# Performance work log

Measured on AMD Instinct MI355X. Metric: run time of the kernel, lower is better.

Reference implementation:

```python
import jax, jax.numpy as jnp
import numpy as np

N_NODES = 50000
N_EDGES = 100000
NODE_IN = 64
EDGE_IN = 16
H = 32          # node_hidden_feats
EDGE_HID = 128  # edge_hidden_feats
STEPS = 6       # num_step_message_passing


def setup_inputs() -> dict:
    key = jax.random.key(0)
    ks = jax.random.split(key, 12)
    s = lambda k, *sh: jax.random.normal(k, sh, dtype=jnp.float32) * 0.05
    return {
        "node_ids": jax.random.randint(ks[0], (N_NODES,), 0, 343),
        "edge_ids": jax.random.randint(ks[1], (N_EDGES,), 0, 21),
        "src": jax.random.randint(ks[2], (N_EDGES,), 0, N_NODES),
        "dst": jax.random.randint(ks[3], (N_EDGES,), 0, N_NODES),
        "node_emb": s(ks[4], 343, NODE_IN),
        "edge_emb": s(ks[5], 21, EDGE_IN),
        "proj_W": s(ks[6], NODE_IN, H),
        "proj_b": jnp.zeros((H,), jnp.float32),
        "eW1": s(ks[7], EDGE_IN, EDGE_HID),
        "eb1": jnp.zeros((EDGE_HID,), jnp.float32),
        "eW2": s(ks[8], EDGE_HID, H * H),
        "eb2": jnp.zeros((H * H,), jnp.float32),
        "conv_bias": jnp.zeros((H,), jnp.float32),
        "gru_Wih": s(ks[9], 3 * H, H),
        "gru_Whh": s(ks[10], 3 * H, H),
        "gru_bih": jnp.zeros((3 * H,), jnp.float32),
        "gru_bhh": jnp.zeros((3 * H,), jnp.float32),
    }


def reference(node_ids, edge_ids, src, dst, node_emb, edge_emb, proj_W, proj_b,
              eW1, eb1, eW2, eb2, conv_bias, gru_Wih, gru_Whh, gru_bih, gru_bhh):
    # project node features
    h = jax.nn.relu(node_emb[node_ids] @ proj_W + proj_b)                 # [N, H]
    e = edge_emb[edge_ids]                                                # [E, EDGE_IN]
    # edge-conditioned weight matrices (edge feats are fixed, so identical every step)
    W_e = (jax.nn.relu(e @ eW1 + eb1) @ eW2 + eb2).reshape(N_EDGES, H, H)  # [E, H, H]
    hidden = h
    for _ in range(STEPS):
        # NNConv: gather src feats, per-edge matvec, scatter-sum to dst, + bias
        msg = jnp.einsum('ei,eio->eo', h[src], W_e)                        # [E, H]
        agg = jax.ops.segment_sum(msg, dst, num_segments=N_NODES) + conv_bias
        m = jax.nn.relu(agg)
        # GRU cell (PyTorch gate order: r, z, n)
        gi = m @ gru_Wih.T + gru_bih                                       # [N, 3H]
        gh = hidden @ gru_Whh.T + gru_bhh                                  # [N, 3H]
        ir, iz, inew = jnp.split(gi, 3, axis=-1)
        hr, hz, hnew = jnp.split(gh, 3, axis=-1)
        r = jax.nn.sigmoid(ir + hr)
        z = jax.nn.sigmoid(iz + hz)
        n = jnp.tanh(inew + r * hnew)
        hidden = (1.0 - z) * n + z * hidden
        h = hidden
    return h
```

## Files before the change

### kernel.cpp

```cpp
#include <hip/hip_runtime.h>

#define N_NODES 50000
#define N_EDGES 100000
#define NT 21
#define STEPS 6
#define BPT 40
#define NB 100
#define EPB 1000

__device__ __forceinline__ float sigm(float x) { return 1.f / (1.f + __expf(-x)); }
__device__ __forceinline__ float tanh_f(float x) {
    float t = __expf(2.f * fabsf(x));
    return copysignf(1.f - 2.f / (t + 1.f), x);
}

__global__ __launch_bounds__(256) void k_proj(const int* __restrict__ node_ids,
                                              const float* __restrict__ node_emb,
                                              const float* __restrict__ W,
                                              const float* __restrict__ b,
                                              float* __restrict__ h) {
    int lane = threadIdx.x & 31;
    int n = blockIdx.x * 8 + (threadIdx.x >> 5);
    if (n >= N_NODES) return;
    float w[64];
#pragma unroll
    for (int i = 0; i < 64; ++i) w[i] = W[i * 32 + lane];
    int id = node_ids[n];
    const float* er = node_emb + id * 64;
    float e0 = er[lane];
    float e1 = er[32 + lane];
    float acc = b[lane];
#pragma unroll
    for (int i = 0; i < 32; ++i) acc += __shfl(e0, i, 32) * w[i];
#pragma unroll
    for (int i = 0; i < 32; ++i) acc += __shfl(e1, i, 32) * w[32 + i];
    h[n * 32 + lane] = fmaxf(acc, 0.f);
}

__global__ __launch_bounds__(128) void k_wtable(const float* __restrict__ edge_emb,
                                                const float* __restrict__ eW1,
                                                const float* __restrict__ eb1,
                                                const float* __restrict__ eW2,
                                                const float* __restrict__ eb2,
                                                float* __restrict__ Wt) {
    __shared__ float x[128];
    int t = blockIdx.x >> 3, c = blockIdx.x & 7;
    int tid = threadIdx.x;
    float acc = eb1[tid];
#pragma unroll
    for (int i = 0; i < 16; ++i) acc += edge_emb[t * 16 + i] * eW1[i * 128 + tid];
    x[tid] = fmaxf(acc, 0.f);
    __syncthreads();
    int j = c * 128 + tid;
    float a = eb2[j];
#pragma unroll 8
    for (int i = 0; i < 128; ++i) a += x[i] * eW2[i * 1024 + j];
    Wt[t * 1024 + j] = a;
}

__global__ __launch_bounds__(256) void k_hist(const int* __restrict__ eid,
                                              int* __restrict__ hist) {
    __shared__ int lc[NT];
    if (threadIdx.x < NT) lc[threadIdx.x] = 0;
    __syncthreads();
    int e0 = blockIdx.x * EPB;
#pragma unroll
    for (int k = 0; k < EPB / 256 + 1; ++k) {
        int e = e0 + k * 256 + threadIdx.x;
        if (e < e0 + EPB) atomicAdd(&lc[eid[e]], 1);
    }
    __syncthreads();
    if (threadIdx.x < NT) hist[blockIdx.x * NT + threadIdx.x] = lc[threadIdx.x];
}

__global__ void k_offs(const int* __restrict__ hist,
                       int* __restrict__ offs,
                       int* __restrict__ cnt,
                       int* __restrict__ base) {
    __shared__ int tot[NT];
    int t = threadIdx.x;
    if (t < NT) {
        int run = 0;
        for (int b = 0; b < NB; ++b) { offs[b * NT + t] = run; run += hist[b * NT + t]; }
        tot[t] = run;
        cnt[t] = run;
    }
    __syncthreads();
    if (t == 0) {
        int r = 0;
        for (int tt = 0; tt < NT; ++tt) { base[tt] = r; r += tot[tt]; }
    }
}

__global__ __launch_bounds__(256) void k_fill2(const int* __restrict__ eid,
                                               const int* __restrict__ offs,
                                               const int* __restrict__ base,
                                               int* __restrict__ perm) {
    __shared__ int cur[NT];
    int b = blockIdx.x;
    if (threadIdx.x < NT) cur[threadIdx.x] = base[threadIdx.x] + offs[b * NT + threadIdx.x];
    __syncthreads();
    int e0 = b * EPB;
#pragma unroll
    for (int k = 0; k < EPB / 256 + 1; ++k) {
        int e = e0 + k * 256 + threadIdx.x;
        if (e < e0 + EPB) {
            int r = atomicAdd(&cur[eid[e]], 1);
            perm[r] = e;
        }
    }
}

__global__ __launch_bounds__(256) void k_msg(const int* __restrict__ perm,
                                             const int* __restrict__ base,
                                             const int* __restrict__ cnt,
                                             const int* __restrict__ src,
                                             const int* __restrict__ dst,
                                             const float* __restrict__ Wt,
                                             const float* __restrict__ h,
                                             float* __restrict__ agg) {
    int t = blockIdx.x / BPT, sub = blockIdx.x % BPT;
    int lane = threadIdx.x & 31, g = threadIdx.x >> 5;
    const float* wp = Wt + t * 1024;
    float w[32];
#pragma unroll
    for (int i = 0; i < 32; ++i) w[i] = wp[i * 32 + lane];
    int n = cnt[t], b0 = base[t];
    for (int idx = sub * 8 + g; idx < n; idx += BPT * 8) {
        int e = perm[b0 + idx];
        int s = src[e], d = dst[e];
        float hv = h[s * 32 + lane];
        float acc = 0.f;
#pragma unroll
        for (int i = 0; i < 32; ++i) acc += __shfl(hv, i, 32) * w[i];
        atomicAdd(&agg[d * 32 + lane], acc);
    }
}

__global__ __launch_bounds__(256) void k_gru(const float* __restrict__ Wih,
                                             const float* __restrict__ Whh,
                                             const float* __restrict__ bih,
                                             const float* __restrict__ bhh,
                                             const float* __restrict__ cb,
                                             float* __restrict__ agg,
                                             float* __restrict__ h) {
    __shared__ float wiT[32 * 96];
    __shared__ float whT[32 * 96];
    for (int u = threadIdx.x; u < 3072; u += 256) {
        int k = u >> 5, i = u & 31;
        wiT[i * 96 + k] = Wih[u];
        whT[i * 96 + k] = Whh[u];
    }
    __syncthreads();
    int gtid = blockIdx.x * 256 + threadIdx.x;
    int n = gtid >> 2, j = gtid & 3;
    if (n >= N_NODES) return;
    float* ap = agg + n * 32;
    float m[32], hv[32];
#pragma unroll
    for (int q = 0; q < 8; ++q) {
        float4 a = ((const float4*)ap)[q];
        float4 c = ((const float4*)cb)[q];
        m[4 * q + 0] = fmaxf(a.x + c.x, 0.f);
        m[4 * q + 1] = fmaxf(a.y + c.y, 0.f);
        m[4 * q + 2] = fmaxf(a.z + c.z, 0.f);
        m[4 * q + 3] = fmaxf(a.w + c.w, 0.f);
    }
#pragma unroll
    for (int q = 0; q < 8; ++q) {
        float4 x = ((const float4*)(h + n * 32))[q];
        hv[4 * q + 0] = x.x; hv[4 * q + 1] = x.y;
        hv[4 * q + 2] = x.z; hv[4 * q + 3] = x.w;
    }
    float4 z4 = make_float4(0.f, 0.f, 0.f, 0.f);
    ((float4*)ap)[2 * j] = z4;
    ((float4*)ap)[2 * j + 1] = z4;

    const int kb = j * 8;
    float acc[8];
#pragma unroll
    for (int q = 0; q < 8; ++q) acc[q] = 0.f;
#pragma unroll
    for (int i = 0; i < 32; ++i) {
        float mi = m[i], hi = hv[i];
        const float* wr = wiT + i * 96 + kb;
        const float* hr = whT + i * 96 + kb;
#pragma unroll
        for (int q = 0; q < 8; ++q) acc[q] += mi * wr[q] + hi * hr[q];
    }
    float rg[8];
#pragma unroll
    for (int q = 0; q < 8; ++q) rg[q] = sigm(acc[q] + bih[kb + q] + bhh[kb + q]);
    float aI[8], aH[8];
#pragma unroll
    for (int q = 0; q < 8; ++q) { aI[q] = 0.f; aH[q] = 0.f; }
#pragma unroll
    for (int i = 0; i < 32; ++i) {
        float mi = m[i], hi = hv[i];
        const float* wr = wiT + i * 96 + 64 + kb;
        const float* hr = whT + i * 96 + 64 + kb;
#pragma unroll
        for (int q = 0; q < 8; ++q) { aI[q] += mi * wr[q]; aH[q] += hi * hr[q]; }
    }
    float nn[8];
#pragma unroll
    for (int q = 0; q < 8; ++q)
        nn[q] = tanh_f(aI[q] + bih[64 + kb + q] + rg[q] * (aH[q] + bhh[64 + kb + q]));
#pragma unroll
    for (int q = 0; q < 8; ++q) acc[q] = 0.f;
#pragma unroll
    for (int i = 0; i < 32; ++i) {
        float mi = m[i], hi = hv[i];
        const float* wr = wiT + i * 96 + 32 + kb;
        const float* hr = whT + i * 96 + 32 + kb;
#pragma unroll
        for (int q = 0; q < 8; ++q) acc[q] += mi * wr[q] + hi * hr[q];
    }
    float out[8];
#pragma unroll
    for (int q = 0; q < 8; ++q) {
        float z = sigm(acc[q] + bih[32 + kb + q] + bhh[32 + kb + q]);
        out[q] = (1.f - z) * nn[q] + z * hv[kb + q];
    }
    float4 o0 = make_float4(out[0], out[1], out[2], out[3]);
    float4 o1 = make_float4(out[4], out[5], out[6], out[7]);
    ((float4*)(h + n * 32 + kb))[0] = o0;
    ((float4*)(h + n * 32 + kb))[1] = o1;
}

extern "C" void kernel_launch(void* const* d_in, const int* in_sizes, int n_in,
                              void* d_out, int out_size, void* d_ws, size_t ws_size,
                              hipStream_t stream) {
    const int*   node_ids  = (const int*)d_in[0];
    const int*   edge_ids  = (const int*)d_in[1];
    const int*   src       = (const int*)d_in[2];
    const int*   dst       = (const int*)d_in[3];
    const float* node_emb  = (const float*)d_in[4];
    const float* edge_emb  = (const float*)d_in[5];
    const float* proj_W    = (const float*)d_in[6];
    const float* proj_b    = (const float*)d_in[7];
    const float* eW1       = (const float*)d_in[8];
    const float* eb1       = (const float*)d_in[9];
    const float* eW2       = (const float*)d_in[10];
    const float* eb2       = (const float*)d_in[11];
    const float* conv_bias = (const float*)d_in[12];
    const float* gWih      = (const float*)d_in[13];
    const float* gWhh      = (const float*)d_in[14];
    const float* gbih      = (const float*)d_in[15];
    const float* gbhh      = (const float*)d_in[16];

    float* h = (float*)d_out;
    char* ws = (char*)d_ws;
    float* agg  = (float*)ws;
    float* Wt   = (float*)(ws + 6400 * 1024);
    int*   hist = (int*)(ws + 6400 * 1024 + 128 * 1024);
    int*   offs = hist + NB * NT;
    int*   cnt  = offs + NB * NT;
    int*   base = cnt + 32;
    int*   perm = base + 32;

    hipMemsetAsync(agg, 0, (size_t)N_NODES * 32 * sizeof(float), stream);

    k_proj<<<(N_NODES + 7) / 8, 256, 0, stream>>>(node_ids, node_emb, proj_W, proj_b, h);
    k_wtable<<<NT * 8, 128, 0, stream>>>(edge_emb, eW1, eb1, eW2, eb2, Wt);
    k_hist<<<NB, 256, 0, stream>>>(edge_ids, hist);
    k_offs<<<1, 64, 0, stream>>>(hist, offs, cnt, base);
    k_fill2<<<NB, 256, 0, stream>>>(edge_ids, offs, base, perm);

    for (int s = 0; s < STEPS; ++s) {
        k_msg<<<NT * BPT, 256, 0, stream>>>(perm, base, cnt, src, dst, Wt, h, agg);
        k_gru<<<(N_NODES * 4 + 255) / 256, 256, 0, stream>>>(gWih, gWhh, gbih, gbhh, conv_bias, agg, h);
    }
}
```

Before: 548.7 us.

## Rewrite GRU kernel as persistent wave with register-resident weights and shuffles

The GRU kernel now launches a fixed grid of single-wave blocks. Each lane owns one output feature and keeps its rows of all six gate weight matrices in registers instead of reading transposed copies from shared memory. Each wave handles two nodes per iteration, broadcasts inputs with shuffles, and prefetches the next pair's agg and h values. This removes the per-block shared-memory staging and the LDS reads, at the cost of about 192 weight registers per lane, which may limit occupancy, and 64 shuffles per node.

Result: slower. 581.8 us (+6.0%).

```diff
diff --git a/kernel.cpp b/kernel.cpp
--- a/kernel.cpp
+++ b/kernel.cpp
@@ -7,6 +7,8 @@
 #define BPT 40
 #define NB 100
 #define EPB 1000
+#define NPAIRS (N_NODES / 2)
+#define GRU_WAVES 2048
 
 __device__ __forceinline__ float sigm(float x) { return 1.f / (1.f + __expf(-x)); }
 __device__ __forceinline__ float tanh_f(float x) {
@@ -137,95 +139,78 @@
     }
 }
 
-__global__ __launch_bounds__(256) void k_gru(const float* __restrict__ Wih,
-                                             const float* __restrict__ Whh,
-                                             const float* __restrict__ bih,
-                                             const float* __restrict__ bhh,
-                                             const float* __restrict__ cb,
-                                             float* __restrict__ agg,
-                                             float* __restrict__ h) {
-    __shared__ float wiT[32 * 96];
-    __shared__ float whT[32 * 96];
-    for (int u = threadIdx.x; u < 3072; u += 256) {
-        int k = u >> 5, i = u & 31;
-        wiT[i * 96 + k] = Wih[u];
-        whT[i * 96 + k] = Whh[u];
-    }
-    __syncthreads();
-    int gtid = blockIdx.x * 256 + threadIdx.x;
-    int n = gtid >> 2, j = gtid & 3;
-    if (n >= N_NODES) return;
-    float* ap = agg + n * 32;
-    float m[32], hv[32];
-#pragma unroll
-    for (int q = 0; q < 8; ++q) {
-        float4 a = ((const float4*)ap)[q];
-        float4 c = ((const float4*)cb)[q];
-        m[4 * q + 0] = fmaxf(a.x + c.x, 0.f);
-        m[4 * q + 1] = fmaxf(a.y + c.y, 0.f);
-        m[4 * q + 2] = fmaxf(a.z + c.z, 0.f);
-        m[4 * q + 3] = fmaxf(a.w + c.w, 0.f);
-    }
-#pragma unroll
-    for (int q = 0; q < 8; ++q) {
-        float4 x = ((const float4*)(h + n * 32))[q];
-        hv[4 * q + 0] = x.x; hv[4 * q + 1] = x.y;
-        hv[4 * q + 2] = x.z; hv[4 * q + 3] = x.w;
-    }
-    float4 z4 = make_float4(0.f, 0.f, 0.f, 0.f);
-    ((float4*)ap)[2 * j] = z4;
-    ((float4*)ap)[2 * j + 1] = z4;
-
-    const int kb = j * 8;
-    float acc[8];
-#pragma unroll
-    for (int q = 0; q < 8; ++q) acc[q] = 0.f;
-#pragma unroll
-    for (int i = 0; i < 32; ++i) {
-        float mi = m[i], hi = hv[i];
-        const float* wr = wiT + i * 96 + kb;
-        const float* hr = whT + i * 96 + kb;
-#pragma unroll
-        for (int q = 0; q < 8; ++q) acc[q] += mi * wr[q] + hi * hr[q];
-    }
-    float rg[8];
-#pragma unroll
-    for (int q = 0; q < 8; ++q) rg[q] = sigm(acc[q] + bih[kb + q] + bhh[kb + q]);
-    float aI[8], aH[8];
-#pragma unroll
-    for (int q = 0; q < 8; ++q) { aI[q] = 0.f; aH[q] = 0.f; }
-#pragma unroll
-    for (int i = 0; i < 32; ++i) {
-        float mi = m[i], hi = hv[i];
-        const float* wr = wiT + i * 96 + 64 + kb;
-        const float* hr = whT + i * 96 + 64 + kb;
-#pragma unroll
-        for (int q = 0; q < 8; ++q) { aI[q] += mi * wr[q]; aH[q] += hi * hr[q]; }
-    }
-    float nn[8];
-#pragma unroll
-    for (int q = 0; q < 8; ++q)
-        nn[q] = tanh_f(aI[q] + bih[64 + kb + q] + rg[q] * (aH[q] + bhh[64 + kb + q]));
-#pragma unroll
-    for (int q = 0; q < 8; ++q) acc[q] = 0.f;
-#pragma unroll
-    for (int i = 0; i < 32; ++i) {
-        float mi = m[i], hi = hv[i];
-        const float* wr = wiT + i * 96 + 32 + kb;
-        const float* hr = whT + i * 96 + 32 + kb;
-#pragma unroll
-        for (int q = 0; q < 8; ++q) acc[q] += mi * wr[q] + hi * hr[q];
-    }
-    float out[8];
-#pragma unroll
-    for (int q = 0; q < 8; ++q) {
-        float z = sigm(acc[q] + bih[32 + kb + q] + bhh[32 + kb + q]);
-        out[q] = (1.f - z) * nn[q] + z * hv[kb + q];
-    }
-    float4 o0 = make_float4(out[0], out[1], out[2], out[3]);
-    float4 o1 = make_float4(out[4], out[5], out[6], out[7]);
-    ((float4*)(h + n * 32 + kb))[0] = o0;
-    ((float4*)(h + n * 32 + kb))[1] = o1;
+__global__ __launch_bounds__(64) void k_gru(const float* __restrict__ Wih,
+                                            const float* __restrict__ Whh,
+                                            const float* __restrict__ bih,
+                                            const float* __restrict__ bhh,
+                                            const float* __restrict__ cb,
+                                            float* __restrict__ agg,
+                                            float* __restrict__ h) {
+    const int lane = threadIdx.x;
+    const int f = lane & 31;
+    const int half = lane >> 5;
+
+    float wiR[32], wiZ[32], wiN[32], whR[32], whZ[32], whN[32];
+    {
+        const float* pR = Wih + f * 32;
+        const float* pZ = Wih + (32 + f) * 32;
+        const float* pN = Wih + (64 + f) * 32;
+        const float* qR = Whh + f * 32;
+        const float* qZ = Whh + (32 + f) * 32;
+        const float* qN = Whh + (64 + f) * 32;
+#pragma unroll
+        for (int c = 0; c < 8; ++c) {
+            float4 a;
+            a = ((const float4*)pR)[c]; wiR[4*c]=a.x; wiR[4*c+1]=a.y; wiR[4*c+2]=a.z; wiR[4*c+3]=a.w;
+            a = ((const float4*)pZ)[c]; wiZ[4*c]=a.x; wiZ[4*c+1]=a.y; wiZ[4*c+2]=a.z; wiZ[4*c+3]=a.w;
+            a = ((const float4*)pN)[c]; wiN[4*c]=a.x; wiN[4*c+1]=a.y; wiN[4*c+2]=a.z; wiN[4*c+3]=a.w;
+            a = ((const float4*)qR)[c]; whR[4*c]=a.x; whR[4*c+1]=a.y; whR[4*c+2]=a.z; whR[4*c+3]=a.w;
+            a = ((const float4*)qZ)[c]; whZ[4*c]=a.x; whZ[4*c+1]=a.y; whZ[4*c+2]=a.z; whZ[4*c+3]=a.w;
+            a = ((const float4*)qN)[c]; whN[4*c]=a.x; whN[4*c+1]=a.y; whN[4*c+2]=a.z; whN[4*c+3]=a.w;
+        }
+    }
+    const float bR  = bih[f] + bhh[f];
+    const float bZ  = bih[32 + f] + bhh[32 + f];
+    const float biN = bih[64 + f];
+    const float bhN = bhh[64 + f];
+    const float cbf = cb[f];
+
+    const int stride = gridDim.x;
+    int p = blockIdx.x;
+    float av = 0.f, hv = 0.f;
+    if (p < NPAIRS) {
+        int n = 2 * p + half;
+        av = agg[n * 32 + f];
+        hv = h[n * 32 + f];
+    }
+    while (p < NPAIRS) {
+        int pn = p + stride;
+        float avN = 0.f, hvN = 0.f;
+        if (pn < NPAIRS) {
+            int nn2 = 2 * pn + half;
+            avN = agg[nn2 * 32 + f];
+            hvN = h[nn2 * 32 + f];
+        }
+        float m = fmaxf(av + cbf, 0.f);
+        float accR = 0.f, accZ = 0.f, accI = 0.f, accH = 0.f;
+#pragma unroll
+        for (int i = 0; i < 32; ++i) {
+            float mi = __shfl(m, i, 32);
+            float hi = __shfl(hv, i, 32);
+            accR += mi * wiR[i] + hi * whR[i];
+            accZ += mi * wiZ[i] + hi * whZ[i];
+            accI += mi * wiN[i];
+            accH += hi * whN[i];
+        }
+        float r = sigm(accR + bR);
+        float z = sigm(accZ + bZ);
+        float nn = tanh_f(accI + biN + r * (accH + bhN));
+        float out = (1.f - z) * nn + z * hv;
+        int n = 2 * p + half;
+        agg[n * 32 + f] = 0.f;
+        h[n * 32 + f] = out;
+        p = pn; av = avN; hv = hvN;
+    }
 }
 
 extern "C" void kernel_launch(void* const* d_in, const int* in_sizes, int n_in,
@@ -269,6 +254,6 @@
 
     for (int s = 0; s < STEPS; ++s) {
         k_msg<<<NT * BPT, 256, 0, stream>>>(perm, base, cnt, src, dst, Wt, h, agg);
-        k_gru<<<(N_NODES * 4 + 255) / 256, 256, 0, stream>>>(gWih, gWhh, gbih, gbhh, conv_bias, agg, h);
-    }
-}
+        k_gru<<<GRU_WAVES, 64, 0, stream>>>(gWih, gWhh, gbih, gbhh, conv_bias, agg, h);
+    }
+}
```
